# Performance work log

Measured on AMD Instinct MI355X. Metric: run time of the kernel, lower is better.

The kernel has to match this reference:

```python
import jax, jax.numpy as jnp
import numpy as np


def _upsample_axis(V, axis):
    """Double size along `axis` by linear interp at half-integer coords with edge clamp.
    out[..., 2i, ...] = V[i]; out[..., 2i+1, ...] = 0.5*(V[i] + V[min(i+1, n-1)])
    This is exactly the SpatialTransformer linear sampling of V at locations f/2.
    """
    n = V.shape[axis]
    last = jax.lax.slice_in_dim(V, n - 1, n, axis=axis)  # clamped edge neighbor
    nxt = jnp.concatenate([jax.lax.slice_in_dim(V, 1, n, axis=axis), last], axis=axis)
    mid = 0.5 * (V + nxt)
    out = jnp.stack([V, mid], axis=axis + 1)  # interleave even/odd samples
    shape = list(V.shape)
    shape[axis] = 2 * n
    return out.reshape(shape)


def setup_inputs() -> dict:
    key = jax.random.key(0)
    V = jax.random.normal(key, (1, 80, 96, 112, 16), dtype=jnp.float32)
    return {"V": V}


def reference(V):
    # V: [B, D1..Dn, C] channels-last volume; upsample every spatial axis by 2
    # via multilinear interpolation (separable since sample coords are axis-aligned
    # half-integers f/2, matching interp_upsampling's identity-grid + (-f/2) offset).
    out = V
    for ax in range(1, V.ndim - 1):
        out = _upsample_axis(out, ax)
    return out
```

## Files before the change

### kernel.cpp

```cpp
#include <hip/hip_runtime.h>


#define DV 80
#define HV 96
#define WV 112
#define ROW4 (WV * 4)
#define OROW4 (2 * WV * 4)

typedef float v4f __attribute__((ext_vector_type(4)));

__device__ __forceinline__ float4 avg4(float4 x, float4 y) {
    return make_float4(0.5f * (x.x + y.x), 0.5f * (x.y + y.y),
                       0.5f * (x.z + y.z), 0.5f * (x.w + y.w));
}

__device__ __forceinline__ void store_nt(float4* p, float4 v) {
    __builtin_nontemporal_store(*reinterpret_cast<const v4f*>(&v),
                                reinterpret_cast<v4f*>(p));
}

__global__ __launch_bounds__(896) void UpsampleInterp_kernel(
        const float4* __restrict__ in, float4* __restrict__ out) {
    const int h0 = blockIdx.x;
    const int d0 = blockIdx.y;
    const int t  = threadIdx.x;
    const int c4 = t & 3;
    const int wo = t >> 2;
    const int wi = wo >> 1;
    const int wodd = wo & 1;
    const int wib = (wi + 1 < WV) ? wi + 1 : WV - 1;
    const int i1 = wodd ? wib : wi;

    const int d1 = (d0 + 1 < DV) ? d0 + 1 : DV - 1;
    const int h1 = (h0 + 1 < HV) ? h0 + 1 : HV - 1;

    const int baseA = (d0 * HV + h0) * ROW4 + c4;
    const int baseB = (d0 * HV + h1) * ROW4 + c4;
    const int baseC = (d1 * HV + h0) * ROW4 + c4;
    const int baseD = (d1 * HV + h1) * ROW4 + c4;

    const float4 A0 = in[baseA + 4 * wi], A1 = in[baseA + 4 * i1];
    const float4 B0 = in[baseB + 4 * wi], B1 = in[baseB + 4 * i1];
    const float4 C0 = in[baseC + 4 * wi], C1 = in[baseC + 4 * i1];
    const float4 D0 = in[baseD + 4 * wi], D1 = in[baseD + 4 * i1];

    const float4 ab0 = avg4(A0, B0), ab1 = avg4(A1, B1);
    const float4 ac0 = avg4(A0, C0), ac1 = avg4(A1, C1);
    const float4 bd0 = avg4(B0, D0), bd1 = avg4(B1, D1);

    const float4 r00 = avg4(A0, A1);
    const float4 r01 = avg4(ab0, ab1);
    const float4 r10 = avg4(ac0, ac1);
    const float4 r11 = avg4(avg4(ac0, bd0), avg4(ac1, bd1));

    const int ob = ((2 * d0) * (2 * HV) + (2 * h0)) * OROW4 + t;
    store_nt(&out[ob],                            r00);
    store_nt(&out[ob + OROW4],                    r01);
    store_nt(&out[ob + (2 * HV) * OROW4],         r10);
    store_nt(&out[ob + (2 * HV) * OROW4 + OROW4], r11);
}

extern "C" void kernel_launch(void* const* d_in, const int* in_sizes, int n_in,
                              void* d_out, int out_size, void* d_ws, size_t ws_size,
                              hipStream_t stream) {
    const float4* in = (const float4*)d_in[0];
    float4* out = (float4*)d_out;
    dim3 grid(HV, DV);
    UpsampleInterp_kernel<<<grid, 896, 0, stream>>>(in, out);
}
```

Measured before the change: 470.2 us.

## Loop each block over a depth strip and reuse loaded input rows

Each block now walks ten consecutive depth slices for one h row and carries the next-depth rows into the following iteration as the current rows. This halves the input loads per output compared with reloading all four neighbouring rows for every depth. The grid shrinks from 7680 to 768 blocks and launch bounds request seven waves per SIMD. In exchange there is less parallelism and a serial dependency chain inside each block. Total output writes are unchanged, and they dominate traffic.

```diff
diff --git a/kernel.cpp b/kernel.cpp
--- a/kernel.cpp
+++ b/kernel.cpp
@@ -4,6 +4,7 @@
 #define DV 80
 #define HV 96
 #define WV 112
+#define KD 10
 #define ROW4 (WV * 4)
 #define OROW4 (2 * WV * 4)
 
@@ -19,45 +20,54 @@
                                 reinterpret_cast<v4f*>(p));
 }
 
-__global__ __launch_bounds__(896) void UpsampleInterp_kernel(
+__global__ __launch_bounds__(896, 7) void UpsampleInterp_kernel(
         const float4* __restrict__ in, float4* __restrict__ out) {
-    const int h0 = blockIdx.x;
-    const int d0 = blockIdx.y;
+    const int bid   = blockIdx.x;
+    const int strip = bid & 7;
+    const int h0    = bid >> 3;
+    const int d0s   = strip * KD;
+
     const int t  = threadIdx.x;
     const int c4 = t & 3;
     const int wo = t >> 2;
     const int wi = wo >> 1;
     const int wodd = wo & 1;
-    const int wib = (wi + 1 < WV) ? wi + 1 : WV - 1;
-    const int i1 = wodd ? wib : wi;
+    const int wib  = (wi + 1 < WV) ? wi + 1 : WV - 1;
+    const int i1   = wodd ? wib : wi;
 
-    const int d1 = (d0 + 1 < DV) ? d0 + 1 : DV - 1;
     const int h1 = (h0 + 1 < HV) ? h0 + 1 : HV - 1;
 
-    const int baseA = (d0 * HV + h0) * ROW4 + c4;
-    const int baseB = (d0 * HV + h1) * ROW4 + c4;
-    const int baseC = (d1 * HV + h0) * ROW4 + c4;
-    const int baseD = (d1 * HV + h1) * ROW4 + c4;
+    const int off0 = c4 + 4 * wi;
+    const int off1 = c4 + 4 * i1;
 
-    const float4 A0 = in[baseA + 4 * wi], A1 = in[baseA + 4 * i1];
-    const float4 B0 = in[baseB + 4 * wi], B1 = in[baseB + 4 * i1];
-    const float4 C0 = in[baseC + 4 * wi], C1 = in[baseC + 4 * i1];
-    const float4 D0 = in[baseD + 4 * wi], D1 = in[baseD + 4 * i1];
+    const int rowA = (d0s * HV + h0) * ROW4;
+    const int rowB = (d0s * HV + h1) * ROW4;
+    float4 A0 = in[rowA + off0], A1 = in[rowA + off1];
+    float4 B0 = in[rowB + off0], B1 = in[rowB + off1];
 
-    const float4 ab0 = avg4(A0, B0), ab1 = avg4(A1, B1);
-    const float4 ac0 = avg4(A0, C0), ac1 = avg4(A1, C1);
-    const float4 bd0 = avg4(B0, D0), bd1 = avg4(B1, D1);
+    int ob = ((2 * d0s) * (2 * HV) + (2 * h0)) * OROW4 + t;
 
-    const float4 r00 = avg4(A0, A1);
-    const float4 r01 = avg4(ab0, ab1);
-    const float4 r10 = avg4(ac0, ac1);
-    const float4 r11 = avg4(avg4(ac0, bd0), avg4(ac1, bd1));
+#pragma unroll 1
+    for (int i = 0; i < KD; ++i) {
+        const int d  = d0s + i;
+        const int d1 = (d + 1 < DV) ? d + 1 : DV - 1;
+        const int rowC = (d1 * HV + h0) * ROW4;
+        const int rowD = (d1 * HV + h1) * ROW4;
+        const float4 C0 = in[rowC + off0], C1 = in[rowC + off1];
+        const float4 D0 = in[rowD + off0], D1 = in[rowD + off1];
 
-    const int ob = ((2 * d0) * (2 * HV) + (2 * h0)) * OROW4 + t;
-    store_nt(&out[ob],                            r00);
-    store_nt(&out[ob + OROW4],                    r01);
-    store_nt(&out[ob + (2 * HV) * OROW4],         r10);
-    store_nt(&out[ob + (2 * HV) * OROW4 + OROW4], r11);
+        const float4 ab0 = avg4(A0, B0), ab1 = avg4(A1, B1);
+        store_nt(&out[ob],         avg4(A0, A1));
+        store_nt(&out[ob + OROW4], avg4(ab0, ab1));
+
+        const float4 ac0 = avg4(A0, C0), ac1 = avg4(A1, C1);
+        const float4 bd0 = avg4(B0, D0), bd1 = avg4(B1, D1);
+        store_nt(&out[ob + (2 * HV) * OROW4],         avg4(ac0, ac1));
+        store_nt(&out[ob + (2 * HV) * OROW4 + OROW4], avg4(avg4(ac0, bd0), avg4(ac1, bd1)));
+
+        A0 = C0; A1 = C1; B0 = D0; B1 = D1;
+        ob += 2 * (2 * HV) * OROW4;
+    }
 }
 
 extern "C" void kernel_launch(void* const* d_in, const int* in_sizes, int n_in,
@@ -65,6 +75,5 @@
                               hipStream_t stream) {
     const float4* in = (const float4*)d_in[0];
     float4* out = (float4*)d_out;
-    dim3 grid(HV, DV);
-    UpsampleInterp_kernel<<<grid, 896, 0, stream>>>(in, out);
+    UpsampleInterp_kernel<<<dim3(HV * (DV / KD)), 896, 0, stream>>>(in, out);
 }
```

New measurement: 484.9 us. 1.03x slower.
